# Optimization experiments

Hardware: AMD Instinct MI355X
Metric: run time of the kernel (lower is better)

Reference implementation:

```python
import jax, jax.numpy as jnp
import numpy as np

DILATION = 6
KS = 3
N = KS * KS  # 9 kernel sample points
PAD = 1      # zero padding inside DeformConv2d
EPS = 1e-5


def conv2d(x, w, b=None, padding=0):
    out = jax.lax.conv_general_dilated(
        x, w, window_strides=(1, 1),
        padding=[(padding, padding), (padding, padding)],
        dimension_numbers=('NCHW', 'OIHW', 'NCHW'))
    if b is not None:
        out = out + b[None, :, None, None]
    return out


def batchnorm_train(x, gamma, beta):
    # training-mode BN (module default): batch statistics over (N,H,W)
    mean = x.mean(axis=(0, 2, 3), keepdims=True)
    var = x.var(axis=(0, 2, 3), keepdims=True)
    return gamma[None, :, None, None] * (x - mean) * jax.lax.rsqrt(var + EPS) + beta[None, :, None, None]


def deform_conv(x, p_w, p_b, m_w, m_b, d_w, d_b, w):
    b, c, h, wd = x.shape
    offset = conv2d(x, p_w, p_b, padding=1)                 # (b, 2N, h, w)
    m = jax.nn.sigmoid(conv2d(x, m_w, m_b, padding=1))      # (b, N, h, w) modulation
    s = 2.0 * jax.nn.sigmoid(conv2d(x, d_w, d_b, padding=1))  # (b,1,h,w) adaptive dilation scale (=1 at logit 0)
    xp = jnp.pad(x, ((0, 0), (0, 0), (PAD, PAD), (PAD, PAD)))
    Hp, Wp = h + 2 * PAD, wd + 2 * PAD
    # kernel grid p_n, row-major (kh, kw) to match conv weight layout
    rng = jnp.arange(-(KS - 1) // 2, (KS - 1) // 2 + 1, dtype=x.dtype)
    pn_x, pn_y = jnp.meshgrid(rng, rng, indexing='ij')
    pn_x, pn_y = pn_x.reshape(-1), pn_y.reshape(-1)          # (N,)
    # base sampling positions (offset by PAD into padded map)
    p0_x = jnp.arange(1, h + 1, dtype=x.dtype)[:, None, None]    # (h,1,1)
    p0_y = jnp.arange(1, wd + 1, dtype=x.dtype)[None, :, None]   # (1,w,1)
    off = offset.transpose(0, 2, 3, 1)   # (b,h,w,2N)
    s_ = s.transpose(0, 2, 3, 1)         # (b,h,w,1)
    px = p0_x + DILATION * s_ * pn_x + off[..., :N]   # (b,h,w,N)
    py = p0_y + DILATION * s_ * pn_y + off[..., N:]
    fx, fy = jnp.floor(px), jnp.floor(py)
    qx_lt = jnp.clip(fx, 0, Hp - 1).astype(jnp.int32)
    qy_lt = jnp.clip(fy, 0, Wp - 1).astype(jnp.int32)
    qx_rb = jnp.clip(fx + 1, 0, Hp - 1).astype(jnp.int32)
    qy_rb = jnp.clip(fy + 1, 0, Wp - 1).astype(jnp.int32)
    pxc = jnp.clip(px, 0, Hp - 1)
    pyc = jnp.clip(py, 0, Wp - 1)
    g_lt = (1 + (qx_lt - pxc)) * (1 + (qy_lt - pyc))
    g_rb = (1 - (qx_rb - pxc)) * (1 - (qy_rb - pyc))
    g_lb = (1 + (qx_lt - pxc)) * (1 - (qy_rb - pyc))
    g_rt = (1 - (qx_rb - pxc)) * (1 + (qy_lt - pyc))

    def gather(qx, qy):
        idx = (qx * Wp + qy).reshape(b, 1, -1)                    # (b,1,h*w*N)
        xf = xp.reshape(b, c, Hp * Wp)
        out = jnp.take_along_axis(xf, jnp.broadcast_to(idx, (b, c, idx.shape[-1])), axis=2)
        return out.reshape(b, c, h, wd, N)

    x_off = (g_lt[:, None] * gather(qx_lt, qy_lt)
             + g_rb[:, None] * gather(qx_rb, qy_rb)
             + g_lb[:, None] * gather(qx_lt, qy_rb)
             + g_rt[:, None] * gather(qx_rb, qy_lt))
    x_off = x_off * m.transpose(0, 2, 3, 1)[:, None]              # modulation
    # final 3x3 conv over gathered samples == contraction over (c, N)
    return jnp.einsum('bchwn,ocn->bohw', x_off, w.reshape(w.shape[0], c, N))


def setup_inputs() -> dict:
    key = jax.random.key(0)
    ks = jax.random.split(key, 12)
    cin, c1, c2 = 512, 256, 64
    b, h, w = 2, 96, 96
    def rn(k, shape, scale):
        return jax.random.normal(k, shape, dtype=jnp.float32) * scale
    return {
        'x': rn(ks[0], (b, cin, h, w), 1.0),
        'bn1_g': jnp.ones((cin,), jnp.float32),
        'bn1_b': jnp.zeros((cin,), jnp.float32),
        'conv1_w': rn(ks[1], (c1, cin, 1, 1), (1.0 / cin) ** 0.5),
        'conv1_b': jnp.zeros((c1,), jnp.float32),
        'bn2_g': jnp.ones((c1,), jnp.float32),
        'bn2_b': jnp.zeros((c1,), jnp.float32),
        'p_w': rn(ks[2], (2 * N, c1, 3, 3), 0.01),
        'p_b': jnp.zeros((2 * N,), jnp.float32),
        'm_w': rn(ks[3], (N, c1, 3, 3), 0.01),
        'm_b': jnp.zeros((N,), jnp.float32),
        'd_w': rn(ks[4], (1, c1, 3, 3), 0.01),
        'd_b': jnp.zeros((1,), jnp.float32),
        'dconv_w': rn(ks[5], (c2, c1, 3, 3), (1.0 / (c1 * 9)) ** 0.5),
    }


def reference(x, bn1_g, bn1_b, conv1_w, conv1_b, bn2_g, bn2_b,
              p_w, p_b, m_w, m_b, d_w, d_b, dconv_w):
    f = jax.nn.relu(batchnorm_train(x, bn1_g, bn1_b))
    f = conv2d(f, conv1_w, conv1_b)
    f = batchnorm_train(f, bn2_g, bn2_b)
    return deform_conv(f, p_w, p_b, m_w, m_b, d_w, d_b, dconv_w)
```

## Files before the change

kernel.cpp:

```cpp
#include <hip/hip_runtime.h>
#include <hip/hip_bf16.h>
#include <math.h>

#define BATCH 2
#define CIN 512
#define C1 256
#define C2 64
#define HH 96
#define WW 96
#define HWSZ 9216
#define NPIX 18432
#define HP 98
#define WP 98
#define PLSTRIDE 516096

typedef __attribute__((ext_vector_type(8))) short bf16x8;
typedef __attribute__((ext_vector_type(4))) short bf16x4;
typedef __attribute__((ext_vector_type(4))) float f32x4;
typedef __attribute__((ext_vector_type(4))) unsigned int u32x4;
typedef __attribute__((ext_vector_type(2))) unsigned int u32x2;
typedef unsigned short u16;
typedef unsigned int u32;

__device__ __forceinline__ float bfu2f(u16 u) {
  u32 v = ((u32)u) << 16; return __builtin_bit_cast(float, v);
}
__device__ __forceinline__ u16 f2bfu(float f) {
  return __builtin_bit_cast(u16, __float2bfloat16(f));
}
__device__ __forceinline__ float rd_any(const void* p, size_t i, int fl) {
  return fl ? bfu2f(((const u16*)p)[i]) : ((const float*)p)[i];
}
__device__ __forceinline__ int get_fl(const u32* g1raw) {
  return g1raw[0] != 0x3F800000u;
}
__device__ __forceinline__ bf16x8 lds_frag(const u16* p) {
  bf16x4 lo = *(const bf16x4*)p;
  bf16x4 hi = *(const bf16x4*)(p + 4);
  bf16x8 r;
  r[0] = lo[0]; r[1] = lo[1]; r[2] = lo[2]; r[3] = lo[3];
  r[4] = hi[0]; r[5] = hi[1]; r[6] = hi[2]; r[7] = hi[3];
  return r;
}
__device__ __forceinline__ void split4(const f32x4& v, u32x2& ph, u32x2& pl) {
  u16 h0 = f2bfu(v[0]), h1 = f2bfu(v[1]), h2 = f2bfu(v[2]), h3 = f2bfu(v[3]);
  u16 l0 = f2bfu(v[0] - bfu2f(h0)), l1 = f2bfu(v[1] - bfu2f(h1));
  u16 l2 = f2bfu(v[2] - bfu2f(h2)), l3 = f2bfu(v[3] - bfu2f(h3));
  ph = (u32x2){(u32)h0 | ((u32)h1 << 16), (u32)h2 | ((u32)h3 << 16)};
  pl = (u32x2){(u32)l0 | ((u32)l1 << 16), (u32)l2 | ((u32)l3 << 16)};
}

__global__ __launch_bounds__(256) void prep_kernel(
    const void* cw, const void* pw, const void* mw, const void* dw, const void* dcw,
    const void* cb, const void* g1, const void* b1, const void* g2, const void* b2,
    const void* pb, const void* mb, const void* db,
    u16* __restrict__ W1b, u16* __restrict__ W1l,
    u16* __restrict__ Wofa, u16* __restrict__ Wofal,
    u16* __restrict__ Wab, u16* __restrict__ Wabl,
    float* __restrict__ canon, float* __restrict__ statz) {
  int e = blockIdx.x * 256 + threadIdx.x;
  if (e >= 356380) return;
  int fl = get_fl((const u32*)g1);
  if (e < 131072) {
    float v = rd_any(cw, e, fl);
    u16 h = f2bfu(v);
    W1b[e] = h; W1l[e] = f2bfu(v - bfu2f(h));
  } else if (e < 204800) {
    int i = e - 131072;
    int tap = i >> 13; int r = i & 8191; int m = r >> 8; int c = r & 255;
    float v = 0.f;
    if (m < 18)       v = rd_any(pw, (size_t)(m * 256 + c) * 9 + tap, fl);
    else if (m < 27)  v = rd_any(mw, (size_t)((m - 18) * 256 + c) * 9 + tap, fl);
    else if (m == 27) v = rd_any(dw, (size_t)c * 9 + tap, fl);
    u16 h = f2bfu(v);
    Wofa[i] = h; Wofal[i] = f2bfu(v - bfu2f(h));
  } else if (e < 352256) {
    int i = e - 204800;
    int n = i >> 14; int r = i & 16383; int o = r >> 8; int c = r & 255;
    float v = rd_any(dcw, (size_t)(o * 256 + c) * 9 + n, fl);
    u16 h = f2bfu(v);
    Wab[i] = h; Wabl[i] = f2bfu(v - bfu2f(h));
  } else if (e < 354076) {
    int i = e - 352256;
    const void* src; int off;
    if      (i < 256)  { src = cb; off = i; }
    else if (i < 768)  { src = g1; off = i - 256; }
    else if (i < 1280) { src = b1; off = i - 768; }
    else if (i < 1536) { src = g2; off = i - 1280; }
    else if (i < 1792) { src = b2; off = i - 1536; }
    else if (i < 1810) { src = pb; off = i - 1792; }
    else if (i < 1819) { src = mb; off = i - 1810; }
    else               { src = db; off = i - 1819; }
    canon[i] = rd_any(src, off, fl);
  } else {
    statz[e - 354076] = 0.f;
  }
}

__global__ __launch_bounds__(256) void bn_stats_kernel(
    const void* __restrict__ x, const float* __restrict__ gamma,
    const float* __restrict__ beta, float* __restrict__ scale,
    float* __restrict__ shift, float* __restrict__ sums, float* __restrict__ sumsq,
    int* __restrict__ cnt, const u32* __restrict__ g1raw, int force, int C) {
  int c = blockIdx.x, part = blockIdx.y, tid = threadIdx.x;
  int fl = force ? 1 : get_fl(g1raw);
  int b = part >> 1, half = part & 1;
  size_t base = ((size_t)(b * C + c)) * HWSZ + half * (HWSZ / 2);
  float s = 0.f, q = 0.f;
  if (fl) {
    const u16* p = (const u16*)x + base;
    for (int i = tid; i < 576; i += 256) {
      u32x4 U = *(const u32x4*)(p + i * 8);
      #pragma unroll
      for (int k = 0; k < 4; ++k) {
        float v0 = bfu2f((u16)(U[k] & 0xffff));
        float v1 = bfu2f((u16)(U[k] >> 16));
        s += v0 + v1; q = fmaf(v0, v0, fmaf(v1, v1, q));
      }
    }
  } else {
    const float* p = (const float*)x + base;
    for (int i = tid; i < 1152; i += 256) {
      f32x4 v = *(const f32x4*)(p + i * 4);
      #pragma unroll
      for (int k = 0; k < 4; ++k) { s += v[k]; q = fmaf(v[k], v[k], q); }
    }
  }
  __shared__ float sh[512];
  sh[tid] = s; sh[tid + 256] = q;
  __syncthreads();
  for (int off = 128; off > 0; off >>= 1) {
    if (tid < off) { sh[tid] += sh[tid + off]; sh[tid + 256] += sh[tid + 256 + off]; }
    __syncthreads();
  }
  if (tid == 0) {
    atomicAdd(&sums[c], sh[0]);
    atomicAdd(&sumsq[c], sh[256]);
    __threadfence();
    int old = atomicAdd(&cnt[c], 1);
    if (old == 3) {
      float S = atomicAdd(&sums[c], 0.f);
      float Q = atomicAdd(&sumsq[c], 0.f);
      float mean = S * (1.f / (float)NPIX);
      float var  = fmaxf(Q * (1.f / (float)NPIX) - mean * mean, 0.f);
      float sc = gamma[c] * rsqrtf(var + 1e-5f);
      scale[c] = sc;
      shift[c] = beta[c] - mean * sc;
    }
  }
}

__global__ __launch_bounds__(256) void conv1x1_kernel(
    const void* __restrict__ x, const u16* __restrict__ W1b, const u16* __restrict__ W1l,
    const float* __restrict__ cb, const float* __restrict__ scale,
    const float* __restrict__ shift, const u32* __restrict__ g1raw,
    u16* __restrict__ f1) {
  __shared__ u16 Bh[2][64][68];
  __shared__ u16 Bl[2][64][68];
  int tid = threadIdx.x;
  int fl = get_fl(g1raw);
  int bxr = blockIdx.x;
  int bx = (bxr & 7) * 36 + (bxr >> 3);
  int p0 = bx * 64;
  int co0 = blockIdx.y * 128;
  int b = p0 / HWSZ;
  int hw0 = p0 % HWSZ;
  int lane = tid & 63, wv = tid >> 6, quad = lane >> 4, mr = lane & 15;
  int m0 = co0 + wv * 32;
  f32x4 acc[2][4];
  #pragma unroll
  for (int i = 0; i < 2; ++i)
    #pragma unroll
    for (int j = 0; j < 4; ++j) acc[i][j] = (f32x4){0.f, 0.f, 0.f, 0.f};

  int spx = tid & 63, cg = tid >> 6;
  int gpx = hw0 + spx;

  float pva[8], pvb[8];
  auto ISSUE = [&](int c0) {
    #pragma unroll
    for (int j = 0; j < 8; ++j) {
      int ci = c0 + cg * 16 + j * 2;
      if (fl) {
        const u16* xb = (const u16*)x;
        pva[j] = bfu2f(xb[((size_t)(b * CIN + ci)) * HWSZ + gpx]);
        pvb[j] = bfu2f(xb[((size_t)(b * CIN + ci + 1)) * HWSZ + gpx]);
      } else {
        const float* xf = (const float*)x;
        pva[j] = xf[((size_t)(b * CIN + ci)) * HWSZ + gpx];
        pvb[j] = xf[((size_t)(b * CIN + ci + 1)) * HWSZ + gpx];
      }
    }
  };
  auto COMBINE = [&](int buf, int c0) {
    #pragma unroll
    for (int j = 0; j < 8; ++j) {
      int ci = c0 + cg * 16 + j * 2;
      float v0 = fmaxf(fmaf(pva[j], scale[ci], shift[ci]), 0.f);
      float v1 = fmaxf(fmaf(pvb[j], scale[ci + 1], shift[ci + 1]), 0.f);
      u16 h0 = f2bfu(v0), h1 = f2bfu(v1);
      u16 l0 = f2bfu(v0 - bfu2f(h0)), l1 = f2bfu(v1 - bfu2f(h1));
      *(u32*)&Bh[buf][spx][cg * 16 + j * 2] = (u32)h0 | ((u32)h1 << 16);
      *(u32*)&Bl[buf][spx][cg * 16 + j * 2] = (u32)l0 | ((u32)l1 << 16);
    }
  };

  ISSUE(0);
  COMBINE(0, 0);
  for (int c8 = 0; c8 < 8; ++c8) {
    __syncthreads();
    if (c8 < 7) ISSUE((c8 + 1) * 64);
    int bsel = c8 & 1;
    int c0 = c8 * 64;
    #pragma unroll
    for (int kk2 = 0; kk2 < 2; ++kk2) {
      int kk = kk2 * 32;
      #pragma unroll
      for (int mf = 0; mf < 2; ++mf) {
        size_t wix = (size_t)(m0 + mf * 16 + mr) * CIN + c0 + kk + quad * 8;
        bf16x8 ah = *(const bf16x8*)(W1b + wix);
        bf16x8 al = *(const bf16x8*)(W1l + wix);
        #pragma unroll
        for (int nt = 0; nt < 4; ++nt) {
          bf16x8 bl = lds_frag(&Bl[bsel][nt * 16 + mr][kk + quad * 8]);
          bf16x8 bh = lds_frag(&Bh[bsel][nt * 16 + mr][kk + quad * 8]);
          acc[mf][nt] = __builtin_amdgcn_mfma_f32_16x16x32_bf16(ah, bl, acc[mf][nt], 0, 0, 0);
          acc[mf][nt] = __builtin_amdgcn_mfma_f32_16x16x32_bf16(al, bh, acc[mf][nt], 0, 0, 0);
          acc[mf][nt] = __builtin_amdgcn_mfma_f32_16x16x32_bf16(ah, bh, acc[mf][nt], 0, 0, 0);
        }
      }
    }
    if (c8 < 7) COMBINE(bsel ^ 1, (c8 + 1) * 64);
  }
  #pragma unroll
  for (int mf = 0; mf < 2; ++mf) {
    #pragma unroll
    for (int nt = 0; nt < 4; ++nt) {
      #pragma unroll
      for (int r = 0; r < 4; ++r) {
        int co = m0 + mf * 16 + quad * 4 + r;
        f1[((size_t)(b * C1 + co)) * HWSZ + hw0 + nt * 16 + mr] = f2bfu(acc[mf][nt][r] + cb[co]);
      }
    }
  }
}

__global__ __launch_bounds__(256) void bn2pad_kernel(
    const u16* __restrict__ f1, const float* __restrict__ scale,
    const float* __restrict__ shift, float* __restrict__ xpf) {
  int bid = blockIdx.x;
  int ht = bid % 144; int ct = (bid / 144) & 3; int b = bid / 576;
  int hw0 = ht * 64, c0 = ct * 64;
  __shared__ float t[64][65];
  int tid = threadIdx.x;
  #pragma unroll
  for (int it = 0; it < 16; ++it) {
    int e = it * 256 + tid;
    int p = e & 63, ci = e >> 6;
    float v = bfu2f(f1[((size_t)(b * C1 + c0 + ci)) * HWSZ + hw0 + p]);
    t[ci][p] = fmaf(v, scale[c0 + ci], shift[c0 + ci]);
  }
  __syncthreads();
  #pragma unroll
  for (int it = 0; it < 16; ++it) {
    int e = it * 256 + tid;
    int ci = e & 63, p = e >> 6;
    int hw = hw0 + p; int h = hw / WW; int w = hw % WW;
    xpf[(((size_t)(b * HP) + h + 1) * WP + w + 1) * C1 + c0 + ci] = t[ci][p];
  }
}

__global__ __launch_bounds__(256) void init_kernel(float* __restrict__ xpf) {
  int k = blockIdx.x * 256 + threadIdx.x;
  int ch = k & 255; int pxi = k >> 8;
  int bb = pxi / 388; int r = pxi % 388;
  int h, w;
  if (r < 98)      { h = 0;  w = r; }
  else if (r < 196){ h = 97; w = r - 98; }
  else if (r < 292){ h = r - 196 + 1; w = 0; }
  else             { h = r - 292 + 1; w = 97; }
  xpf[(((size_t)(bb * HP) + h) * WP + w) * C1 + ch] = 0.f;
}

__global__ __launch_bounds__(256) void offconv_kernel(
    const float* __restrict__ xpf, const u16* __restrict__ Wofa, const u16* __restrict__ Wofal,
    const float* __restrict__ pbc, const float* __restrict__ mbc,
    const float* __restrict__ dbc, float* __restrict__ opart3) {
  __shared__ u16 Vh[2][32][68];
  __shared__ u16 Vl[2][32][68];
  int tid = threadIdx.x;
  int bxr = blockIdx.x;
  int bx = (bxr & 7) * 72 + (bxr >> 3);
  int tg = blockIdx.y;
  int p0 = bx * 32;
  int b = p0 / HWSZ;
  int hw = p0 % HWSZ; int h0 = hw / WW; int w0 = hw % WW;
  int lane = tid & 63, wv = tid >> 6, quad = lane >> 4, mr = lane & 15;
  int m0 = (wv & 1) * 16;
  int ntile = wv >> 1;
  int srow = tid >> 4;
  int scol = (tid & 15) * 4;
  f32x4 acc = (f32x4){0.f, 0.f, 0.f, 0.f};

  f32x4 pv[2];
  auto ISSUE = [&](int it) {
    int tap = tg * 3 + (it >> 2);
    int th = tap / 3, tw = tap % 3;
    int c0 = (it & 3) * 64;
    const float* base = xpf + ((size_t)(b * HP + h0 + th) * WP + (w0 + tw)) * C1;
    #pragma unroll
    for (int pass = 0; pass < 2; ++pass) {
      int px = pass * 16 + srow;
      pv[pass] = *(const f32x4*)(base + (size_t)px * C1 + c0 + scol);
    }
  };
  auto COMBINE = [&](int buf) {
    #pragma unroll
    for (int pass = 0; pass < 2; ++pass) {
      int px = pass * 16 + srow;
      u32x2 ph, pl;
      split4(pv[pass], ph, pl);
      *(u32x2*)&Vh[buf][px][scol] = ph;
      *(u32x2*)&Vl[buf][px][scol] = pl;
    }
  };

  ISSUE(0);
  COMBINE(0);
  for (int it = 0; it < 12; ++it) {
    __syncthreads();
    if (it < 11) ISSUE(it + 1);
    int bsel = it & 1;
    int tap = tg * 3 + (it >> 2);
    int c0 = (it & 3) * 64;
    #pragma unroll
    for (int kk2 = 0; kk2 < 2; ++kk2) {
      int kof = kk2 * 32 + quad * 8;
      size_t wix = (size_t)(tap * 32 + m0 + mr) * C1 + c0 + kof;
      bf16x8 ah = *(const bf16x8*)(Wofa + wix);
      bf16x8 al = *(const bf16x8*)(Wofal + wix);
      bf16x8 bl = lds_frag(&Vl[bsel][ntile * 16 + mr][kof]);
      bf16x8 bh = lds_frag(&Vh[bsel][ntile * 16 + mr][kof]);
      acc = __builtin_amdgcn_mfma_f32_16x16x32_bf16(ah, bl, acc, 0, 0, 0);
      acc = __builtin_amdgcn_mfma_f32_16x16x32_bf16(al, bh, acc, 0, 0, 0);
      acc = __builtin_amdgcn_mfma_f32_16x16x32_bf16(ah, bh, acc, 0, 0, 0);
    }
    if (it < 11) COMBINE(bsel ^ 1);
  }
  float* plane = opart3 + (size_t)tg * PLSTRIDE;
  int px = ntile * 16 + mr;
  #pragma unroll
  for (int r = 0; r < 4; ++r) {
    int m = m0 + quad * 4 + r;
    if (m < 28) {
      float v = acc[r];
      if (tg == 0) v += (m < 18) ? pbc[m] : ((m < 27) ? mbc[m - 18] : dbc[0]);
      plane[(size_t)m * NPIX + p0 + px] = v;
    }
  }
}

__global__ __launch_bounds__(256) void deform_kernel(
    const float* __restrict__ xpf, const u16* __restrict__ Wab, const u16* __restrict__ Wabl,
    const float* __restrict__ opart3, const u32* __restrict__ g1raw,
    void* __restrict__ outv) {
  __shared__ u16   Vh[2][32][68];
  __shared__ u16   Vl[2][32][68];
  __shared__ int   smi[9][4][32];
  __shared__ float smw[9][4][32];
  int tid = threadIdx.x;
  int bxr = blockIdx.x;
  int bx = (bxr & 7) * 72 + (bxr >> 3);
  int p0 = bx * 32;
  int b = p0 / HWSZ;
  int hw0 = p0 % HWSZ;

  for (int e = tid; e < 288; e += 256) {
    int n = e >> 5;
    int p = e & 31;
    int bp = p0 + p;
    int hw = hw0 + p; int h = hw / WW; int w = hw % WW;
    const float* P0 = opart3;
    const float* P1 = opart3 + PLSTRIDE;
    const float* P2 = opart3 + 2 * PLSTRIDE;
    size_t iox = (size_t)n * NPIX + bp;
    size_t ioy = (size_t)(9 + n) * NPIX + bp;
    size_t iml = (size_t)(18 + n) * NPIX + bp;
    size_t isl = (size_t)27 * NPIX + bp;
    float offx = P0[iox] + P1[iox] + P2[iox];
    float offy = P0[ioy] + P1[ioy] + P2[ioy];
    float mlog = P0[iml] + P1[iml] + P2[iml];
    float slog = P0[isl] + P1[isl] + P2[isl];
    float mm = 1.f / (1.f + expf(-mlog));
    float s  = 2.f / (1.f + expf(-slog));
    float pnx = (float)(n / 3 - 1), pny = (float)(n % 3 - 1);
    float px = (float)(h + 1) + 6.f * s * pnx + offx;
    float py = (float)(w + 1) + 6.f * s * pny + offy;
    float fx = floorf(px), fy = floorf(py);
    float qxlt = fminf(fmaxf(fx, 0.f), 97.f);
    float qylt = fminf(fmaxf(fy, 0.f), 97.f);
    float qxrb = fminf(fmaxf(fx + 1.f, 0.f), 97.f);
    float qyrb = fminf(fmaxf(fy + 1.f, 0.f), 97.f);
    float pxc = fminf(fmaxf(px, 0.f), 97.f);
    float pyc = fminf(fmaxf(py, 0.f), 97.f);
    float glt = (1.f + (qxlt - pxc)) * (1.f + (qylt - pyc));
    float grb = (1.f - (qxrb - pxc)) * (1.f - (qyrb - pyc));
    float glb = (1.f + (qxlt - pxc)) * (1.f - (qyrb - pyc));
    float grt = (1.f - (qxrb - pxc)) * (1.f + (qylt - pyc));
    int ixlt = (int)qxlt, iylt = (int)qylt, ixrb = (int)qxrb, iyrb = (int)qyrb;
    int base = b * (HP * WP);
    smi[n][0][p] = base + ixlt * WP + iylt;  smw[n][0][p] = glt * mm;
    smi[n][1][p] = base + ixrb * WP + iyrb;  smw[n][1][p] = grb * mm;
    smi[n][2][p] = base + ixlt * WP + iyrb;  smw[n][2][p] = glb * mm;
    smi[n][3][p] = base + ixrb * WP + iylt;  smw[n][3][p] = grt * mm;
  }
  __syncthreads();

  int lane = tid & 63, wv = tid >> 6, quad = lane >> 4, mr = lane & 15;
  int m0 = wv * 16;
  int srow = tid >> 4;
  int scol = (tid & 15) * 4;
  f32x4 acc[2];
  acc[0] = (f32x4){0.f, 0.f, 0.f, 0.f};
  acc[1] = (f32x4){0.f, 0.f, 0.f, 0.f};

  f32x4 pv[2][4];
  auto ISSUE = [&](int it) {
    int n = it >> 2; int c0 = (it & 3) * 64;
    #pragma unroll
    for (int pass = 0; pass < 2; ++pass) {
      int px = pass * 16 + srow;
      #pragma unroll
      for (int k = 0; k < 4; ++k)
        pv[pass][k] = *(const f32x4*)(xpf + (size_t)smi[n][k][px] * C1 + c0 + scol);
    }
  };
  auto COMBINE = [&](int buf, int it) {
    int n = it >> 2;
    #pragma unroll
    for (int pass = 0; pass < 2; ++pass) {
      int px = pass * 16 + srow;
      float w0 = smw[n][0][px], w1 = smw[n][1][px], w2 = smw[n][2][px], w3 = smw[n][3][px];
      f32x4 vc;
      #pragma unroll
      for (int j = 0; j < 4; ++j)
        vc[j] = fmaf(w0, pv[pass][0][j],
                fmaf(w1, pv[pass][1][j],
                fmaf(w2, pv[pass][2][j], w3 * pv[pass][3][j])));
      u32x2 ph, pl;
      split4(vc, ph, pl);
      *(u32x2*)&Vh[buf][px][scol] = ph;
      *(u32x2*)&Vl[buf][px][scol] = pl;
    }
  };

  ISSUE(0);
  COMBINE(0, 0);
  for (int it = 0; it < 36; ++it) {
    __syncthreads();
    if (it < 35) ISSUE(it + 1);
    int bsel = it & 1;
    int n = it >> 2; int c0 = (it & 3) * 64;
    #pragma unroll
    for (int kk2 = 0; kk2 < 2; ++kk2) {
      int kof = kk2 * 32 + quad * 8;
      size_t wix = (size_t)(n * C2 + m0 + mr) * C1 + c0 + kof;
      bf16x8 ah = *(const bf16x8*)(Wab + wix);
      bf16x8 al = *(const bf16x8*)(Wabl + wix);
      #pragma unroll
      for (int nt = 0; nt < 2; ++nt) {
        bf16x8 bl = lds_frag(&Vl[bsel][nt * 16 + mr][kof]);
        bf16x8 bh = lds_frag(&Vh[bsel][nt * 16 + mr][kof]);
        acc[nt] = __builtin_amdgcn_mfma_f32_16x16x32_bf16(ah, bl, acc[nt], 0, 0, 0);
        acc[nt] = __builtin_amdgcn_mfma_f32_16x16x32_bf16(al, bh, acc[nt], 0, 0, 0);
        acc[nt] = __builtin_amdgcn_mfma_f32_16x16x32_bf16(ah, bh, acc[nt], 0, 0, 0);
      }
    }
    if (it < 35) COMBINE(bsel ^ 1, it + 1);
  }
  int fl = get_fl(g1raw);
  #pragma unroll
  for (int nt = 0; nt < 2; ++nt) {
    #pragma unroll
    for (int r = 0; r < 4; ++r) {
      int o = m0 + quad * 4 + r;
      int hw = hw0 + nt * 16 + mr;
      size_t oi = ((size_t)(b * C2 + o)) * HWSZ + hw;
      if (fl) ((u16*)outv)[oi] = f2bfu(acc[nt][r]);
      else    ((float*)outv)[oi] = acc[nt][r];
    }
  }
}

extern "C" void kernel_launch(void* const* d_in, const int* in_sizes, int n_in,
                              void* d_out, int out_size, void* d_ws, size_t ws_size,
                              hipStream_t stream) {
  const void* x       = d_in[0];
  const void* bn1_g   = d_in[1];
  const void* bn1_b   = d_in[2];
  const void* conv1_w = d_in[3];
  const void* conv1_b = d_in[4];
  const void* bn2_g   = d_in[5];
  const void* bn2_b   = d_in[6];
  const void* p_w     = d_in[7];
  const void* p_b     = d_in[8];
  const void* m_w     = d_in[9];
  const void* m_b     = d_in[10];
  const void* d_w     = d_in[11];
  const void* d_b     = d_in[12];
  const void* dconv_w = d_in[13];
  const u32* g1raw = (const u32*)bn1_g;

  float* ws = (float*)d_ws;
  float* canon = ws + 16;
  float* cbc = canon + 0;
  float* g1c = canon + 256;
  float* b1c = canon + 768;
  float* g2c = canon + 1280;
  float* b2c = canon + 1536;
  float* pbc = canon + 1792;
  float* mbc = canon + 1810;
  float* dbc = canon + 1819;
  float* scale1 = ws + 1840;
  float* shift1 = ws + 2352;
  float* scale2 = ws + 2864;
  float* shift2 = ws + 3120;
  float* statz  = ws + 3376;
  float* sums1  = statz;
  float* sumsq1 = statz + 512;
  int*   cnt1   = (int*)(statz + 1024);
  float* sums2  = statz + 1536;
  float* sumsq2 = statz + 1792;
  int*   cnt2   = (int*)(statz + 2048);
  u16* W1b   = (u16*)(ws + 5680);
  u16* W1l   = (u16*)(ws + 71216);
  u16* Wofa  = (u16*)(ws + 136752);
  u16* Wofal = (u16*)(ws + 173616);
  u16* Wab   = (u16*)(ws + 210480);
  u16* Wabl  = (u16*)(ws + 284208);
  u16* f1    = (u16*)(ws + 357936);
  float* opart3 = ws + 357936;
  float* xpf   = ws + 2717232;

  prep_kernel<<<1393, 256, 0, stream>>>(conv1_w, p_w, m_w, d_w, dconv_w,
                                        conv1_b, bn1_g, bn1_b, bn2_g, bn2_b,
                                        p_b, m_b, d_b,
                                        W1b, W1l, Wofa, Wofal, Wab, Wabl, canon, statz);
  bn_stats_kernel<<<dim3(CIN, 4), 256, 0, stream>>>(x, g1c, b1c, scale1, shift1,
                                                    sums1, sumsq1, cnt1, g1raw, 0, CIN);
  conv1x1_kernel<<<dim3(288, 2), 256, 0, stream>>>(x, W1b, W1l, cbc, scale1, shift1, g1raw, f1);
  bn_stats_kernel<<<dim3(C1, 4), 256, 0, stream>>>(f1, g2c, b2c, scale2, shift2,
                                                   sums2, sumsq2, cnt2, g1raw, 1, C1);
  bn2pad_kernel<<<1152, 256, 0, stream>>>(f1, scale2, shift2, xpf);
  init_kernel<<<776, 256, 0, stream>>>(xpf);
  offconv_kernel<<<dim3(576, 3), 256, 0, stream>>>(xpf, Wofa, Wofal, pbc, mbc, dbc, opart3);
  deform_kernel<<<576, 256, 0, stream>>>(xpf, Wab, Wabl, opart3, g1raw, d_out);
}
```

Before: 332.6 us.

## Split deform conv over kernel-point groups and gather directly into MFMA registers

The deform kernel is restructured so that each block handles 64 pixels and one of three groups of kernel sample points. Each lane computes its own bilinear indices and weights and gathers samples straight into MFMA A-operand registers, which removes the LDS staging and the barriers. The three partial planes are summed by a new reduce kernel, at the cost of extra global traffic and one more launch. Separately, the conv1x1 pixel tile is halved to 32 and the grid doubled, which raises parallelism but weakens weight reuse.

```diff
diff --git a/kernel.cpp b/kernel.cpp
--- a/kernel.cpp
+++ b/kernel.cpp
@@ -155,32 +155,32 @@
     const float* __restrict__ cb, const float* __restrict__ scale,
     const float* __restrict__ shift, const u32* __restrict__ g1raw,
     u16* __restrict__ f1) {
-  __shared__ u16 Bh[2][64][68];
-  __shared__ u16 Bl[2][64][68];
+  __shared__ u16 Bh[2][32][68];
+  __shared__ u16 Bl[2][32][68];
   int tid = threadIdx.x;
   int fl = get_fl(g1raw);
   int bxr = blockIdx.x;
-  int bx = (bxr & 7) * 36 + (bxr >> 3);
-  int p0 = bx * 64;
+  int bx = (bxr & 7) * 72 + (bxr >> 3);
+  int p0 = bx * 32;
   int co0 = blockIdx.y * 128;
   int b = p0 / HWSZ;
   int hw0 = p0 % HWSZ;
   int lane = tid & 63, wv = tid >> 6, quad = lane >> 4, mr = lane & 15;
   int m0 = co0 + wv * 32;
-  f32x4 acc[2][4];
+  f32x4 acc[2][2];
   #pragma unroll
   for (int i = 0; i < 2; ++i)
     #pragma unroll
-    for (int j = 0; j < 4; ++j) acc[i][j] = (f32x4){0.f, 0.f, 0.f, 0.f};
-
-  int spx = tid & 63, cg = tid >> 6;
+    for (int j = 0; j < 2; ++j) acc[i][j] = (f32x4){0.f, 0.f, 0.f, 0.f};
+
+  int spx = tid & 31, cg = tid >> 5;
   int gpx = hw0 + spx;
 
-  float pva[8], pvb[8];
+  float pva[4], pvb[4];
   auto ISSUE = [&](int c0) {
     #pragma unroll
-    for (int j = 0; j < 8; ++j) {
-      int ci = c0 + cg * 16 + j * 2;
+    for (int j = 0; j < 4; ++j) {
+      int ci = c0 + cg * 8 + j * 2;
       if (fl) {
         const u16* xb = (const u16*)x;
         pva[j] = bfu2f(xb[((size_t)(b * CIN + ci)) * HWSZ + gpx]);
@@ -194,14 +194,14 @@
   };
   auto COMBINE = [&](int buf, int c0) {
     #pragma unroll
-    for (int j = 0; j < 8; ++j) {
-      int ci = c0 + cg * 16 + j * 2;
+    for (int j = 0; j < 4; ++j) {
+      int ci = c0 + cg * 8 + j * 2;
       float v0 = fmaxf(fmaf(pva[j], scale[ci], shift[ci]), 0.f);
       float v1 = fmaxf(fmaf(pvb[j], scale[ci + 1], shift[ci + 1]), 0.f);
       u16 h0 = f2bfu(v0), h1 = f2bfu(v1);
       u16 l0 = f2bfu(v0 - bfu2f(h0)), l1 = f2bfu(v1 - bfu2f(h1));
-      *(u32*)&Bh[buf][spx][cg * 16 + j * 2] = (u32)h0 | ((u32)h1 << 16);
-      *(u32*)&Bl[buf][spx][cg * 16 + j * 2] = (u32)l0 | ((u32)l1 << 16);
+      *(u32*)&Bh[buf][spx][cg * 8 + j * 2] = (u32)h0 | ((u32)h1 << 16);
+      *(u32*)&Bl[buf][spx][cg * 8 + j * 2] = (u32)l0 | ((u32)l1 << 16);
     }
   };
 
@@ -221,7 +221,7 @@
         bf16x8 ah = *(const bf16x8*)(W1b + wix);
         bf16x8 al = *(const bf16x8*)(W1l + wix);
         #pragma unroll
-        for (int nt = 0; nt < 4; ++nt) {
+        for (int nt = 0; nt < 2; ++nt) {
           bf16x8 bl = lds_frag(&Bl[bsel][nt * 16 + mr][kk + quad * 8]);
           bf16x8 bh = lds_frag(&Bh[bsel][nt * 16 + mr][kk + quad * 8]);
           acc[mf][nt] = __builtin_amdgcn_mfma_f32_16x16x32_bf16(ah, bl, acc[mf][nt], 0, 0, 0);
@@ -235,7 +235,7 @@
   #pragma unroll
   for (int mf = 0; mf < 2; ++mf) {
     #pragma unroll
-    for (int nt = 0; nt < 4; ++nt) {
+    for (int nt = 0; nt < 2; ++nt) {
       #pragma unroll
       for (int r = 0; r < 4; ++r) {
         int co = m0 + mf * 16 + quad * 4 + r;
@@ -360,39 +360,39 @@
   }
 }
 
-__global__ __launch_bounds__(256) void deform_kernel(
+__global__ __launch_bounds__(256, 4) void deform_kernel(
     const float* __restrict__ xpf, const u16* __restrict__ Wab, const u16* __restrict__ Wabl,
-    const float* __restrict__ opart3, const u32* __restrict__ g1raw,
-    void* __restrict__ outv) {
-  __shared__ u16   Vh[2][32][68];
-  __shared__ u16   Vl[2][32][68];
-  __shared__ int   smi[9][4][32];
-  __shared__ float smw[9][4][32];
+    const float* __restrict__ opart3, float* __restrict__ planes3) {
   int tid = threadIdx.x;
   int bxr = blockIdx.x;
-  int bx = (bxr & 7) * 72 + (bxr >> 3);
-  int p0 = bx * 32;
+  int bx = (bxr & 7) * 36 + (bxr >> 3);
+  int g = blockIdx.y;
+  int wv = tid >> 6, lane = tid & 63, mr = lane & 15, quad = lane >> 4;
+  int p0 = bx * 64 + wv * 16;
   int b = p0 / HWSZ;
-  int hw0 = p0 % HWSZ;
-
-  for (int e = tid; e < 288; e += 256) {
-    int n = e >> 5;
-    int p = e & 31;
-    int bp = p0 + p;
-    int hw = hw0 + p; int h = hw / WW; int w = hw % WW;
-    const float* P0 = opart3;
-    const float* P1 = opart3 + PLSTRIDE;
-    const float* P2 = opart3 + 2 * PLSTRIDE;
-    size_t iox = (size_t)n * NPIX + bp;
-    size_t ioy = (size_t)(9 + n) * NPIX + bp;
-    size_t iml = (size_t)(18 + n) * NPIX + bp;
-    size_t isl = (size_t)27 * NPIX + bp;
+  int p = p0 + mr;
+  int hw = p % HWSZ; int h = hw / WW; int w = hw % WW;
+
+  const float* P0 = opart3;
+  const float* P1 = opart3 + PLSTRIDE;
+  const float* P2 = opart3 + 2 * PLSTRIDE;
+  size_t isl = (size_t)27 * NPIX + p;
+  float slog = P0[isl] + P1[isl] + P2[isl];
+  float s = 2.f / (1.f + expf(-slog));
+  int pbase = b * (HP * WP);
+
+  int  cidx[3][4];
+  float cwt[3][4];
+  #pragma unroll
+  for (int nn = 0; nn < 3; ++nn) {
+    int n = g * 3 + nn;
+    size_t iox = (size_t)n * NPIX + p;
+    size_t ioy = (size_t)(9 + n) * NPIX + p;
+    size_t iml = (size_t)(18 + n) * NPIX + p;
     float offx = P0[iox] + P1[iox] + P2[iox];
     float offy = P0[ioy] + P1[ioy] + P2[ioy];
     float mlog = P0[iml] + P1[iml] + P2[iml];
-    float slog = P0[isl] + P1[isl] + P2[isl];
     float mm = 1.f / (1.f + expf(-mlog));
-    float s  = 2.f / (1.f + expf(-slog));
     float pnx = (float)(n / 3 - 1), pny = (float)(n % 3 - 1);
     float px = (float)(h + 1) + 6.f * s * pnx + offx;
     float py = (float)(w + 1) + 6.f * s * pny + offy;
@@ -408,87 +408,86 @@
     float glb = (1.f + (qxlt - pxc)) * (1.f - (qyrb - pyc));
     float grt = (1.f - (qxrb - pxc)) * (1.f + (qylt - pyc));
     int ixlt = (int)qxlt, iylt = (int)qylt, ixrb = (int)qxrb, iyrb = (int)qyrb;
-    int base = b * (HP * WP);
-    smi[n][0][p] = base + ixlt * WP + iylt;  smw[n][0][p] = glt * mm;
-    smi[n][1][p] = base + ixrb * WP + iyrb;  smw[n][1][p] = grb * mm;
-    smi[n][2][p] = base + ixlt * WP + iyrb;  smw[n][2][p] = glb * mm;
-    smi[n][3][p] = base + ixrb * WP + iylt;  smw[n][3][p] = grt * mm;
-  }
-  __syncthreads();
-
-  int lane = tid & 63, wv = tid >> 6, quad = lane >> 4, mr = lane & 15;
-  int m0 = wv * 16;
-  int srow = tid >> 4;
-  int scol = (tid & 15) * 4;
-  f32x4 acc[2];
-  acc[0] = (f32x4){0.f, 0.f, 0.f, 0.f};
-  acc[1] = (f32x4){0.f, 0.f, 0.f, 0.f};
-
-  f32x4 pv[2][4];
-  auto ISSUE = [&](int it) {
-    int n = it >> 2; int c0 = (it & 3) * 64;
-    #pragma unroll
-    for (int pass = 0; pass < 2; ++pass) {
-      int px = pass * 16 + srow;
+    cidx[nn][0] = (pbase + ixlt * WP + iylt) * C1;  cwt[nn][0] = glt * mm;
+    cidx[nn][1] = (pbase + ixrb * WP + iyrb) * C1;  cwt[nn][1] = grb * mm;
+    cidx[nn][2] = (pbase + ixlt * WP + iyrb) * C1;  cwt[nn][2] = glb * mm;
+    cidx[nn][3] = (pbase + ixrb * WP + iylt) * C1;  cwt[nn][3] = grt * mm;
+  }
+
+  f32x4 acc[4];
+  #pragma unroll
+  for (int i = 0; i < 4; ++i) acc[i] = (f32x4){0.f, 0.f, 0.f, 0.f};
+
+  #pragma unroll
+  for (int nn = 0; nn < 3; ++nn) {
+    int n = g * 3 + nn;
+    float w0 = cwt[nn][0], w1 = cwt[nn][1], w2 = cwt[nn][2], w3 = cwt[nn][3];
+    #pragma unroll
+    for (int c0i = 0; c0i < 4; ++c0i) {
       #pragma unroll
-      for (int k = 0; k < 4; ++k)
-        pv[pass][k] = *(const f32x4*)(xpf + (size_t)smi[n][k][px] * C1 + c0 + scol);
-    }
-  };
-  auto COMBINE = [&](int buf, int it) {
-    int n = it >> 2;
-    #pragma unroll
-    for (int pass = 0; pass < 2; ++pass) {
-      int px = pass * 16 + srow;
-      float w0 = smw[n][0][px], w1 = smw[n][1][px], w2 = smw[n][2][px], w3 = smw[n][3][px];
-      f32x4 vc;
-      #pragma unroll
-      for (int j = 0; j < 4; ++j)
-        vc[j] = fmaf(w0, pv[pass][0][j],
-                fmaf(w1, pv[pass][1][j],
-                fmaf(w2, pv[pass][2][j], w3 * pv[pass][3][j])));
-      u32x2 ph, pl;
-      split4(vc, ph, pl);
-      *(u32x2*)&Vh[buf][px][scol] = ph;
-      *(u32x2*)&Vl[buf][px][scol] = pl;
-    }
-  };
-
-  ISSUE(0);
-  COMBINE(0, 0);
-  for (int it = 0; it < 36; ++it) {
-    __syncthreads();
-    if (it < 35) ISSUE(it + 1);
-    int bsel = it & 1;
-    int n = it >> 2; int c0 = (it & 3) * 64;
-    #pragma unroll
-    for (int kk2 = 0; kk2 < 2; ++kk2) {
-      int kof = kk2 * 32 + quad * 8;
-      size_t wix = (size_t)(n * C2 + m0 + mr) * C1 + c0 + kof;
-      bf16x8 ah = *(const bf16x8*)(Wab + wix);
-      bf16x8 al = *(const bf16x8*)(Wabl + wix);
-      #pragma unroll
-      for (int nt = 0; nt < 2; ++nt) {
-        bf16x8 bl = lds_frag(&Vl[bsel][nt * 16 + mr][kof]);
-        bf16x8 bh = lds_frag(&Vh[bsel][nt * 16 + mr][kof]);
-        acc[nt] = __builtin_amdgcn_mfma_f32_16x16x32_bf16(ah, bl, acc[nt], 0, 0, 0);
-        acc[nt] = __builtin_amdgcn_mfma_f32_16x16x32_bf16(al, bh, acc[nt], 0, 0, 0);
-        acc[nt] = __builtin_amdgcn_mfma_f32_16x16x32_bf16(ah, bh, acc[nt], 0, 0, 0);
+      for (int kk2 = 0; kk2 < 2; ++kk2) {
+        int ch0 = c0i * 64 + kk2 * 32 + quad * 8;
+        f32x4 ga[4], gb[4];
+        #pragma unroll
+        for (int k = 0; k < 4; ++k) {
+          const float* src = xpf + (size_t)cidx[nn][k] + ch0;
+          ga[k] = *(const f32x4*)src;
+          gb[k] = *(const f32x4*)(src + 4);
+        }
+        bf16x8 ah, al;
+        #pragma unroll
+        for (int j = 0; j < 4; ++j) {
+          float v = fmaf(w0, ga[0][j], fmaf(w1, ga[1][j], fmaf(w2, ga[2][j], w3 * ga[3][j])));
+          u16 hh = f2bfu(v);
+          ah[j] = (short)hh; al[j] = (short)f2bfu(v - bfu2f(hh));
+        }
+        #pragma unroll
+        for (int j = 0; j < 4; ++j) {
+          float v = fmaf(w0, gb[0][j], fmaf(w1, gb[1][j], fmaf(w2, gb[2][j], w3 * gb[3][j])));
+          u16 hh = f2bfu(v);
+          ah[4 + j] = (short)hh; al[4 + j] = (short)f2bfu(v - bfu2f(hh));
+        }
+        #pragma unroll
+        for (int cb = 0; cb < 4; ++cb) {
+          size_t wix = (size_t)(n * C2 + cb * 16 + mr) * C1 + ch0;
+          bf16x8 wh = *(const bf16x8*)(Wab + wix);
+          bf16x8 wl = *(const bf16x8*)(Wabl + wix);
+          acc[cb] = __builtin_amdgcn_mfma_f32_16x16x32_bf16(ah, wl, acc[cb], 0, 0, 0);
+          acc[cb] = __builtin_amdgcn_mfma_f32_16x16x32_bf16(al, wh, acc[cb], 0, 0, 0);
+          acc[cb] = __builtin_amdgcn_mfma_f32_16x16x32_bf16(ah, wh, acc[cb], 0, 0, 0);
+        }
       }
     }
-    if (it < 35) COMBINE(bsel ^ 1, it + 1);
-  }
-  int fl = get_fl(g1raw);
-  #pragma unroll
-  for (int nt = 0; nt < 2; ++nt) {
-    #pragma unroll
-    for (int r = 0; r < 4; ++r) {
-      int o = m0 + quad * 4 + r;
-      int hw = hw0 + nt * 16 + mr;
-      size_t oi = ((size_t)(b * C2 + o)) * HWSZ + hw;
-      if (fl) ((u16*)outv)[oi] = f2bfu(acc[nt][r]);
-      else    ((float*)outv)[oi] = acc[nt][r];
-    }
+  }
+  #pragma unroll
+  for (int cb = 0; cb < 4; ++cb) {
+    int co = cb * 16 + mr;
+    *(f32x4*)(planes3 + ((size_t)g * C2 + co) * NPIX + p0 + quad * 4) = acc[cb];
+  }
+}
+
+__global__ __launch_bounds__(256) void reduce_kernel(
+    const float* __restrict__ planes3, const u32* __restrict__ g1raw,
+    void* __restrict__ outv) {
+  int t = blockIdx.x * 256 + threadIdx.x;
+  int e4 = t * 4;
+  int b = e4 / (C2 * HWSZ);
+  int rem = e4 % (C2 * HWSZ);
+  int o = rem / HWSZ;
+  int hw = rem % HWSZ;
+  size_t src = (size_t)o * NPIX + b * HWSZ + hw;
+  f32x4 v0 = *(const f32x4*)(planes3 + src);
+  f32x4 v1 = *(const f32x4*)(planes3 + (size_t)C2 * NPIX + src);
+  f32x4 v2 = *(const f32x4*)(planes3 + 2 * (size_t)C2 * NPIX + src);
+  f32x4 sum;
+  #pragma unroll
+  for (int j = 0; j < 4; ++j) sum[j] = v0[j] + v1[j] + v2[j];
+  if (get_fl(g1raw)) {
+    u16* ob = (u16*)outv;
+    #pragma unroll
+    for (int j = 0; j < 4; ++j) ob[e4 + j] = f2bfu(sum[j]);
+  } else {
+    *(f32x4*)((float*)outv + e4) = sum;
   }
 }
 
@@ -540,7 +539,8 @@
   u16* Wabl  = (u16*)(ws + 284208);
   u16* f1    = (u16*)(ws + 357936);
   float* opart3 = ws + 357936;
-  float* xpf   = ws + 2717232;
+  float* xpf    = ws + 2717232;
+  float* planes3 = ws + 7634480;
 
   prep_kernel<<<1393, 256, 0, stream>>>(conv1_w, p_w, m_w, d_w, dconv_w,
                                         conv1_b, bn1_g, bn1_b, bn2_g, bn2_b,
@@ -548,11 +548,12 @@
                                         W1b, W1l, Wofa, Wofal, Wab, Wabl, canon, statz);
   bn_stats_kernel<<<dim3(CIN, 4), 256, 0, stream>>>(x, g1c, b1c, scale1, shift1,
                                                     sums1, sumsq1, cnt1, g1raw, 0, CIN);
-  conv1x1_kernel<<<dim3(288, 2), 256, 0, stream>>>(x, W1b, W1l, cbc, scale1, shift1, g1raw, f1);
+  conv1x1_kernel<<<dim3(576, 2), 256, 0, stream>>>(x, W1b, W1l, cbc, scale1, shift1, g1raw, f1);
   bn_stats_kernel<<<dim3(C1, 4), 256, 0, stream>>>(f1, g2c, b2c, scale2, shift2,
                                                    sums2, sumsq2, cnt2, g1raw, 1, C1);
   bn2pad_kernel<<<1152, 256, 0, stream>>>(f1, scale2, shift2, xpf);
   init_kernel<<<776, 256, 0, stream>>>(xpf);
   offconv_kernel<<<dim3(576, 3), 256, 0, stream>>>(xpf, Wofa, Wofal, pbc, mbc, dbc, opart3);
-  deform_kernel<<<576, 256, 0, stream>>>(xpf, Wab, Wabl, opart3, g1raw, d_out);
-}
+  deform_kernel<<<dim3(288, 3), 256, 0, stream>>>(xpf, Wab, Wabl, opart3, planes3);
+  reduce_kernel<<<1152, 256, 0, stream>>>(planes3, g1raw, d_out);
+}
```

New measurement: 440.6 us. +32.5%, slower.

## Split deform conv over kernel taps into three partial planes plus reduce kernel

Applied to the files above, without the earlier changes.

The deform kernel is split along the 9 sampling points into 3 groups of 3, launched as a 576x3 grid. Each block accumulates a partial sum into its own fp32 plane, and a new reduce kernel adds the three planes and writes the output in bf16 or fp32. This triples the block count, so occupancy improves on a 576-block grid that underfills the GPU. In exchange it adds a kernel launch, writes and reads the partial planes, and recomputes per-pixel setup for each group.

```diff
diff --git a/kernel.cpp b/kernel.cpp
--- a/kernel.cpp
+++ b/kernel.cpp
@@ -362,22 +362,23 @@
 
 __global__ __launch_bounds__(256) void deform_kernel(
     const float* __restrict__ xpf, const u16* __restrict__ Wab, const u16* __restrict__ Wabl,
-    const float* __restrict__ opart3, const u32* __restrict__ g1raw,
-    void* __restrict__ outv) {
+    const float* __restrict__ opart3, float* __restrict__ planes3) {
   __shared__ u16   Vh[2][32][68];
   __shared__ u16   Vl[2][32][68];
-  __shared__ int   smi[9][4][32];
-  __shared__ float smw[9][4][32];
+  __shared__ int   smi[3][4][32];
+  __shared__ float smw[3][4][32];
   int tid = threadIdx.x;
   int bxr = blockIdx.x;
   int bx = (bxr & 7) * 72 + (bxr >> 3);
+  int g = blockIdx.y;
   int p0 = bx * 32;
   int b = p0 / HWSZ;
   int hw0 = p0 % HWSZ;
 
-  for (int e = tid; e < 288; e += 256) {
-    int n = e >> 5;
-    int p = e & 31;
+  if (tid < 96) {
+    int nn = tid >> 5;
+    int p = tid & 31;
+    int n = g * 3 + nn;
     int bp = p0 + p;
     int hw = hw0 + p; int h = hw / WW; int w = hw % WW;
     const float* P0 = opart3;
@@ -409,10 +410,10 @@
     float grt = (1.f - (qxrb - pxc)) * (1.f + (qylt - pyc));
     int ixlt = (int)qxlt, iylt = (int)qylt, ixrb = (int)qxrb, iyrb = (int)qyrb;
     int base = b * (HP * WP);
-    smi[n][0][p] = base + ixlt * WP + iylt;  smw[n][0][p] = glt * mm;
-    smi[n][1][p] = base + ixrb * WP + iyrb;  smw[n][1][p] = grb * mm;
-    smi[n][2][p] = base + ixlt * WP + iyrb;  smw[n][2][p] = glb * mm;
-    smi[n][3][p] = base + ixrb * WP + iylt;  smw[n][3][p] = grt * mm;
+    smi[nn][0][p] = base + ixlt * WP + iylt;  smw[nn][0][p] = glt * mm;
+    smi[nn][1][p] = base + ixrb * WP + iyrb;  smw[nn][1][p] = grb * mm;
+    smi[nn][2][p] = base + ixlt * WP + iyrb;  smw[nn][2][p] = glb * mm;
+    smi[nn][3][p] = base + ixrb * WP + iylt;  smw[nn][3][p] = grt * mm;
   }
   __syncthreads();
 
@@ -426,21 +427,21 @@
 
   f32x4 pv[2][4];
   auto ISSUE = [&](int it) {
-    int n = it >> 2; int c0 = (it & 3) * 64;
+    int nn = it >> 2; int c0 = (it & 3) * 64;
     #pragma unroll
     for (int pass = 0; pass < 2; ++pass) {
       int px = pass * 16 + srow;
       #pragma unroll
       for (int k = 0; k < 4; ++k)
-        pv[pass][k] = *(const f32x4*)(xpf + (size_t)smi[n][k][px] * C1 + c0 + scol);
+        pv[pass][k] = *(const f32x4*)(xpf + (size_t)smi[nn][k][px] * C1 + c0 + scol);
     }
   };
   auto COMBINE = [&](int buf, int it) {
-    int n = it >> 2;
+    int nn = it >> 2;
     #pragma unroll
     for (int pass = 0; pass < 2; ++pass) {
       int px = pass * 16 + srow;
-      float w0 = smw[n][0][px], w1 = smw[n][1][px], w2 = smw[n][2][px], w3 = smw[n][3][px];
+      float w0 = smw[nn][0][px], w1 = smw[nn][1][px], w2 = smw[nn][2][px], w3 = smw[nn][3][px];
       f32x4 vc;
       #pragma unroll
       for (int j = 0; j < 4; ++j)
@@ -456,11 +457,11 @@
 
   ISSUE(0);
   COMBINE(0, 0);
-  for (int it = 0; it < 36; ++it) {
+  for (int it = 0; it < 12; ++it) {
     __syncthreads();
-    if (it < 35) ISSUE(it + 1);
+    if (it < 11) ISSUE(it + 1);
     int bsel = it & 1;
-    int n = it >> 2; int c0 = (it & 3) * 64;
+    int n = g * 3 + (it >> 2); int c0 = (it & 3) * 64;
     #pragma unroll
     for (int kk2 = 0; kk2 < 2; ++kk2) {
       int kof = kk2 * 32 + quad * 8;
@@ -476,19 +477,40 @@
         acc[nt] = __builtin_amdgcn_mfma_f32_16x16x32_bf16(ah, bh, acc[nt], 0, 0, 0);
       }
     }
-    if (it < 35) COMBINE(bsel ^ 1, it + 1);
-  }
-  int fl = get_fl(g1raw);
+    if (it < 11) COMBINE(bsel ^ 1, it + 1);
+  }
   #pragma unroll
   for (int nt = 0; nt < 2; ++nt) {
     #pragma unroll
     for (int r = 0; r < 4; ++r) {
       int o = m0 + quad * 4 + r;
-      int hw = hw0 + nt * 16 + mr;
-      size_t oi = ((size_t)(b * C2 + o)) * HWSZ + hw;
-      if (fl) ((u16*)outv)[oi] = f2bfu(acc[nt][r]);
-      else    ((float*)outv)[oi] = acc[nt][r];
-    }
+      planes3[((size_t)g * C2 + o) * NPIX + p0 + nt * 16 + mr] = acc[nt][r];
+    }
+  }
+}
+
+__global__ __launch_bounds__(256) void reduce_kernel(
+    const float* __restrict__ planes3, const u32* __restrict__ g1raw,
+    void* __restrict__ outv) {
+  int t = blockIdx.x * 256 + threadIdx.x;
+  int e4 = t * 4;
+  int b = e4 / (C2 * HWSZ);
+  int rem = e4 % (C2 * HWSZ);
+  int o = rem / HWSZ;
+  int hw = rem % HWSZ;
+  size_t src = (size_t)o * NPIX + b * HWSZ + hw;
+  f32x4 v0 = *(const f32x4*)(planes3 + src);
+  f32x4 v1 = *(const f32x4*)(planes3 + (size_t)C2 * NPIX + src);
+  f32x4 v2 = *(const f32x4*)(planes3 + 2 * (size_t)C2 * NPIX + src);
+  f32x4 sum;
+  #pragma unroll
+  for (int j = 0; j < 4; ++j) sum[j] = v0[j] + v1[j] + v2[j];
+  if (get_fl(g1raw)) {
+    u16* ob = (u16*)outv;
+    #pragma unroll
+    for (int j = 0; j < 4; ++j) ob[e4 + j] = f2bfu(sum[j]);
+  } else {
+    *(f32x4*)((float*)outv + e4) = sum;
   }
 }
 
@@ -540,7 +562,8 @@
   u16* Wabl  = (u16*)(ws + 284208);
   u16* f1    = (u16*)(ws + 357936);
   float* opart3 = ws + 357936;
-  float* xpf   = ws + 2717232;
+  float* xpf    = ws + 2717232;
+  float* planes3 = ws + 7634480;
 
   prep_kernel<<<1393, 256, 0, stream>>>(conv1_w, p_w, m_w, d_w, dconv_w,
                                         conv1_b, bn1_g, bn1_b, bn2_g, bn2_b,
@@ -554,5 +577,6 @@
   bn2pad_kernel<<<1152, 256, 0, stream>>>(f1, scale2, shift2, xpf);
   init_kernel<<<776, 256, 0, stream>>>(xpf);
   offconv_kernel<<<dim3(576, 3), 256, 0, stream>>>(xpf, Wofa, Wofal, pbc, mbc, dbc, opart3);
-  deform_kernel<<<576, 256, 0, stream>>>(xpf, Wab, Wabl, opart3, g1raw, d_out);
-}
+  deform_kernel<<<dim3(576, 3), 256, 0, stream>>>(xpf, Wab, Wabl, opart3, planes3);
+  reduce_kernel<<<1152, 256, 0, stream>>>(planes3, g1raw, d_out);
+}
```

Result: faster. 323.2 us (-2.8%).
